# Performance work log

Hardware: AMD Instinct MI355X
Metric: run time of the kernel (lower is better)

## Reference

```python
import jax, jax.numpy as jnp
import numpy as np

EPS = 1e-10            # safe_log epsilon
SIGMOID_BETA = 1.0
MLE_STEP_SIZE = 0.01
NUM_MLE_STEPS = 15
ENT_MULT = 0.01        # entropy loss multiplier placeholder
DECAY_MULT = 0.001     # weight decay multiplier placeholder
B, P, N, T = 512, 1024, 1024, 32


def sigmoid(a, beta=SIGMOID_BETA):
    # module's rescaled sigmoid: 2/(1+exp(-beta*a)) - 1, range (-1, 1)
    return 2.0 / (1.0 + jnp.exp(-beta * a)) - 1.0


def tri_basis(a_sig, centers):
    # triangle basis functions: relu(1 - |a - c_j| / width), width = center spacing
    # a_sig [B,N], centers [T] -> [B,N,T]
    width = centers[1] - centers[0]
    return jax.nn.relu(1.0 - jnp.abs(a_sig[..., None] - centers) / width)


def prob_est(a_sig, thetas, centers):
    # per-neuron mixture of triangle kernels; mixture weights = softmax(thetas)
    pi = jax.nn.softmax(thetas, axis=1)               # [N,T]
    return jnp.einsum('bnt,nt->bn', tri_basis(a_sig, centers), pi)  # [B,N]


def log_likelihood(a_sig, thetas, centers):
    return jnp.sum(jnp.log(prob_est(a_sig, thetas, centers) + EPS))


def calc_entropy(probs):
    # per-neuron entropy reduction over the batch axis
    return -jnp.sum(probs * jnp.log(probs + EPS), axis=0)  # [N]


def setup_inputs() -> dict:
    key = jax.random.key(0)
    k0, k1, k2, k3 = jax.random.split(key, 4)
    x = jax.random.normal(k0, (B, P), jnp.float32)
    w_enc = 0.5 * jax.random.normal(k1, (P, N), jnp.float32)   # truncated_normal std 0.5 approx
    b_enc = 0.1 * jax.random.normal(k2, (N,), jnp.float32)
    w_dec = jnp.transpose(w_enc)                                # initialized as w_enc^T
    b_dec = 0.1 * jax.random.normal(k3, (P,), jnp.float32)
    thetas = jnp.ones((N, T), jnp.float32)                      # construct_thetas init
    triangle_centers = jnp.linspace(-1.0, 1.0, T).astype(jnp.float32)  # a_sig range
    return {"x": x, "w_enc": w_enc, "b_enc": b_enc, "w_dec": w_dec,
            "b_dec": b_dec, "thetas": thetas, "triangle_centers": triangle_centers}


def reference(x, w_enc, b_enc, w_dec, b_dec, thetas, triangle_centers):
    # --- inference: relu encoder (noise_var_mult = 0 -> deterministic a) ---
    a = jax.nn.relu(x @ w_enc + b_enc)                # [B,N]
    a_sig = sigmoid(a, SIGMOID_BETA)                  # [B,N] in (-1,1)

    # --- iterative MLE gradient-ascent on thetas (num_mle_steps updates) ---
    ll_grad = jax.grad(lambda th: log_likelihood(a_sig, th, triangle_centers))

    def mle_step(th, _):
        return th + MLE_STEP_SIZE * ll_grad(th), None

    thetas_new, _ = jax.lax.scan(mle_step, thetas, None, length=NUM_MLE_STEPS)

    # --- entropy of the triangle-kernel density estimate ---
    probs = prob_est(a_sig, thetas_new, triangle_centers)   # [B,N]
    a_entropies = calc_entropy(probs)                       # [N]

    # --- decoder / losses ---
    x_hat = a @ w_dec + b_dec                               # [B,P]
    recon_loss = jnp.mean(0.5 * jnp.sum((x - x_hat) ** 2, axis=1))
    entropy_loss = ENT_MULT * jnp.sum(a_entropies)
    # tf.nn.l2_loss(t) = sum(t^2)/2
    decay_loss = 0.5 * DECAY_MULT * (0.5 * jnp.sum(w_enc ** 2) + 0.5 * jnp.sum(w_dec ** 2))
    total_loss = recon_loss + entropy_loss + decay_loss
    return x_hat, a_entropies, total_loss
```

## Files before the change

kernel.cpp:

```cpp
#include <hip/hip_runtime.h>

#define EPSC 1e-10f
#define BDIM 512
#define PDIM 1024
#define NDIM 1024
#define TDIM 32

typedef __attribute__((ext_vector_type(8))) short short8;
typedef __attribute__((ext_vector_type(4))) float f32x4;
typedef __attribute__((ext_vector_type(2))) int int2v;

static __device__ __forceinline__ short f2bf(float f) {
  unsigned u = __float_as_uint(f);
  unsigned r = (u + 0x7fffu + ((u >> 16) & 1u)) >> 16;
  return (short)r;
}

template <int CTRL>
static __device__ __forceinline__ float dpp_add(float x) {
  int t = __builtin_amdgcn_update_dpp(0, __float_as_int(x), CTRL, 0xf, 0xf, true);
  return x + __int_as_float(t);
}
static __device__ __forceinline__ float sum16_all(float x) {
  x = dpp_add<0xB1>(x);
  x = dpp_add<0x4E>(x);
  x = dpp_add<0x141>(x);
  x = dpp_add<0x140>(x);
  return x;
}
static __device__ __forceinline__ float sum32_all(float x) {
  x = sum16_all(x);
  int2v r = __builtin_amdgcn_permlane16_swap(__float_as_int(x), __float_as_int(x), false, false);
  return __int_as_float(r[0]) + __int_as_float(r[1]);
}
static __device__ __forceinline__ float sum64_all(float x) {
  x = sum32_all(x);
  int2v r = __builtin_amdgcn_permlane32_swap(__float_as_int(x), __float_as_int(x), false, false);
  return __int_as_float(r[0]) + __int_as_float(r[1]);
}

__global__ __launch_bounds__(256) void conv_kernel(
    const float* __restrict__ X, short* __restrict__ Xbf,
    const float* __restrict__ W1, const float* __restrict__ W2,
    short* __restrict__ T1, short* __restrict__ T2, float* __restrict__ accums)
{
  __shared__ float T[64][65];
  __shared__ float red[4];
  int tid = threadIdx.x;
  int bid = blockIdx.x;
  if (bid < 256) {
    size_t base = (size_t)bid * 2048 + (size_t)tid * 8;
    float4 v0 = *(const float4*)(X + base);
    float4 v1 = *(const float4*)(X + base + 4);
    short8 o;
    o[0] = f2bf(v0.x); o[1] = f2bf(v0.y); o[2] = f2bf(v0.z); o[3] = f2bf(v0.w);
    o[4] = f2bf(v1.x); o[5] = f2bf(v1.y); o[6] = f2bf(v1.z); o[7] = f2bf(v1.w);
    *(short8*)(Xbf + base) = o;
    return;
  }
  int wbid = bid - 256;
  int z = wbid >> 8;
  int rem = wbid & 255;
  int r0 = (rem >> 4) * 64;
  int c0 = (rem & 15) * 64;
  const float* src = z ? W2 : W1;
  short* dst = z ? T2 : T1;
  float wsq = 0.0f;
#pragma unroll
  for (int i = 0; i < 4; ++i) {
    int row = (tid >> 4) + i * 16;
    int col = (tid & 15) << 2;
    float4 v = *(const float4*)(src + (size_t)(r0 + row) * NDIM + c0 + col);
    T[row][col + 0] = v.x; T[row][col + 1] = v.y; T[row][col + 2] = v.z; T[row][col + 3] = v.w;
    wsq = fmaf(v.x, v.x, wsq); wsq = fmaf(v.y, v.y, wsq);
    wsq = fmaf(v.z, v.z, wsq); wsq = fmaf(v.w, v.w, wsq);
  }
  __syncthreads();
  int n = tid >> 2;
  int kb = (tid & 3) << 4;
  short8 o0, o1;
#pragma unroll
  for (int i = 0; i < 8; ++i) o0[i] = f2bf(T[kb + i][n]);
#pragma unroll
  for (int i = 0; i < 8; ++i) o1[i] = f2bf(T[kb + 8 + i][n]);
  short* dp = dst + (size_t)(c0 + n) * NDIM + r0 + kb;
  *(short8*)dp = o0;
  *(short8*)(dp + 8) = o1;
  wsq = sum64_all(wsq);
  if ((tid & 63) == 0) red[tid >> 6] = wsq;
  __syncthreads();
  if (tid == 0) atomicAdd(accums + 2, red[0] + red[1] + red[2] + red[3]);
}

__global__ __launch_bounds__(512) void gemm1_mfma(
    const short* __restrict__ Xbf, const short* __restrict__ WT,
    const float* __restrict__ bias, const float* __restrict__ centers,
    short* __restrict__ Abf, float* __restrict__ U)
{
  __shared__ float red[4][64][9];
  int tid = threadIdx.x;
  int lane = tid & 63, wid = tid >> 6;
  int ow = wid & 3, kz = wid >> 2;
  int q = lane >> 4, r16 = lane & 15;
  int bn = blockIdx.x * 32;
  int m = blockIdx.y * 64 + ow * 16 + r16;
  const short* ap  = Xbf + (size_t)m * NDIM + kz * 512 + q * 8;
  const short* b0p = WT + (size_t)(bn + r16) * NDIM + kz * 512 + q * 8;
  const short* b1p = b0p + 16 * NDIM;
  f32x4 acc0 = {0.f, 0.f, 0.f, 0.f};
  f32x4 acc1 = {0.f, 0.f, 0.f, 0.f};
#pragma unroll 4
  for (int k = 0; k < 512; k += 32) {
    short8 a  = *(const short8*)(ap + k);
    short8 b0 = *(const short8*)(b0p + k);
    short8 b1 = *(const short8*)(b1p + k);
    acc0 = __builtin_amdgcn_mfma_f32_16x16x32_bf16(a, b0, acc0, 0, 0, 0);
    acc1 = __builtin_amdgcn_mfma_f32_16x16x32_bf16(a, b1, acc1, 0, 0, 0);
  }
  if (kz) {
#pragma unroll
    for (int r = 0; r < 4; ++r) { red[ow][lane][r] = acc0[r]; red[ow][lane][r + 4] = acc1[r]; }
  }
  __syncthreads();
  if (!kz) {
#pragma unroll
    for (int r = 0; r < 4; ++r) { acc0[r] += red[ow][lane][r]; acc1[r] += red[ow][lane][r + 4]; }
    float c0v = centers[0];
    float invw = 1.0f / (centers[1] - centers[0]);
    int mrow = blockIdx.y * 64 + ow * 16 + (q << 2);
    int n0 = bn + r16;
    float bi0 = bias[n0], bi1 = bias[n0 + 16];
    float u0[4], u1[4];
#pragma unroll
    for (int r = 0; r < 4; ++r) {
      int mm = mrow + r;
      float a0 = fmaxf(acc0[r] + bi0, 0.0f);
      float a1 = fmaxf(acc1[r] + bi1, 0.0f);
      Abf[(size_t)mm * NDIM + n0]      = f2bf(a0);
      Abf[(size_t)mm * NDIM + n0 + 16] = f2bf(a1);
      u0[r] = (2.0f * __builtin_amdgcn_rcpf(1.0f + __expf(-a0)) - 1.0f - c0v) * invw;
      u1[r] = (2.0f * __builtin_amdgcn_rcpf(1.0f + __expf(-a1)) - 1.0f - c0v) * invw;
    }
    *(float4*)(U + (size_t)n0 * BDIM + mrow)          = *(float4*)u0;
    *(float4*)(U + (size_t)(n0 + 16) * BDIM + mrow)   = *(float4*)u1;
  }
}

__global__ __launch_bounds__(512) void fused2_kernel(
    const short* __restrict__ Abf, const short* __restrict__ WdT,
    const float* __restrict__ b_dec, const float* __restrict__ X,
    const float* __restrict__ U, const float* __restrict__ thetas,
    float* __restrict__ out, float* __restrict__ ent_out, float* __restrict__ accums)
{
  __shared__ float smem[2312];
  int tid = threadIdx.x;
  int bx = blockIdx.x;
  if (bx < 256) {
    int lane = tid & 63, wid = tid >> 6;
    int ow = wid & 3, kz = wid >> 2;
    int q = lane >> 4, r16 = lane & 15;
    int bn = (bx & 31) * 32;
    int by = bx >> 5;
    int m = by * 64 + ow * 16 + r16;
    const short* ap  = Abf + (size_t)m * NDIM + kz * 512 + q * 8;
    const short* b0p = WdT + (size_t)(bn + r16) * NDIM + kz * 512 + q * 8;
    const short* b1p = b0p + 16 * NDIM;
    f32x4 acc0 = {0.f, 0.f, 0.f, 0.f};
    f32x4 acc1 = {0.f, 0.f, 0.f, 0.f};
#pragma unroll 4
    for (int k = 0; k < 512; k += 32) {
      short8 a  = *(const short8*)(ap + k);
      short8 b0 = *(const short8*)(b0p + k);
      short8 b1 = *(const short8*)(b1p + k);
      acc0 = __builtin_amdgcn_mfma_f32_16x16x32_bf16(a, b0, acc0, 0, 0, 0);
      acc1 = __builtin_amdgcn_mfma_f32_16x16x32_bf16(a, b1, acc1, 0, 0, 0);
    }
    float* rw = smem + ((ow * 64 + lane) * 9);
    if (kz) {
#pragma unroll
      for (int r = 0; r < 4; ++r) { rw[r] = acc0[r]; rw[r + 4] = acc1[r]; }
    }
    __syncthreads();
    float local = 0.0f;
    if (!kz) {
#pragma unroll
      for (int r = 0; r < 4; ++r) { acc0[r] += rw[r]; acc1[r] += rw[r + 4]; }
      int mrow = by * 64 + ow * 16 + (q << 2);
      int p0 = bn + r16;
      float bi0 = b_dec[p0], bi1 = b_dec[p0 + 16];
#pragma unroll
      for (int r = 0; r < 4; ++r) {
        int mm = mrow + r;
        float xh0 = acc0[r] + bi0;
        float xh1 = acc1[r] + bi1;
        out[(size_t)mm * PDIM + p0]      = xh0;
        out[(size_t)mm * PDIM + p0 + 16] = xh1;
        float d0 = xh0 - X[(size_t)mm * PDIM + p0];
        float d1 = xh1 - X[(size_t)mm * PDIM + p0 + 16];
        local = fmaf(d0, d0, local);
        local = fmaf(d1, d1, local);
      }
    }
    local = sum64_all(local);
    if ((tid & 63) == 0) smem[2304 + wid] = local;
    __syncthreads();
    if (tid == 0) {
      float s = 0.0f;
#pragma unroll
      for (int i = 0; i < 8; ++i) s += smem[2304 + i];
      atomicAdd(accums + 0, s);
    }
  } else {
    int wid = tid >> 6, lane = tid & 63;
    int n = (bx - 256) * 8 + wid;
    const float* Un = U + (size_t)n * BDIM;
    float u_reg[8], f_reg[8];
    int j_reg[8];
#pragma unroll
    for (int i = 0; i < 8; ++i) {
      float u = Un[lane + i * 64];
      int j = (int)u;
      if (j > TDIM - 2) j = TDIM - 2;
      u_reg[i] = u;
      j_reg[i] = j;
      f_reg[i] = u - (float)j;
    }
    float tv = thetas[(size_t)n * TDIM + (lane & 31)];
    int t = lane & 31;
    for (int step = 0; step < 15; ++step) {
      float e = __expf(tv - 1.0f);
      float se = sum32_all(e);
      float pv = e * __builtin_amdgcn_rcpf(se);
      float S = 0.0f;
      float cs[17];
#pragma unroll
      for (int k = 0; k < 17; ++k) cs[k] = 0.0f;
#pragma unroll
      for (int i = 0; i < 8; ++i) {
        float pj  = __shfl(pv, j_reg[i]);
        float pj1 = __shfl(pv, j_reg[i] + 1);
        float p = fmaf(f_reg[i], pj1 - pj, pj);
        float r = __builtin_amdgcn_rcpf(p + EPSC);
        S = fmaf(p, r, S);
        float u = u_reg[i];
#pragma unroll
        for (int k = 0; k < 17; ++k) {
          float w = __saturatef(1.0f - fabsf(u - (float)(15 + k)));
          cs[k] = fmaf(w, r, cs[k]);
        }
      }
      S = sum64_all(S);
#pragma unroll
      for (int k = 0; k < 17; ++k) cs[k] = sum64_all(cs[k]);
      float colsum = 0.0f;
#pragma unroll
      for (int k = 0; k < 17; ++k) colsum = (t == 15 + k) ? cs[k] : colsum;
      if (lane < 32) tv += 0.01f * pv * (colsum - S);
    }
    float e = __expf(tv - 1.0f);
    float se = sum32_all(e);
    float pv = e * __builtin_amdgcn_rcpf(se);
    float ent_local = 0.0f;
#pragma unroll
    for (int i = 0; i < 8; ++i) {
      float pj  = __shfl(pv, j_reg[i]);
      float pj1 = __shfl(pv, j_reg[i] + 1);
      float p = fmaf(f_reg[i], pj1 - pj, pj);
      ent_local = fmaf(p, __logf(p + EPSC), ent_local);
    }
    float E = sum64_all(ent_local);
    if (lane == 0) {
      float entn = -E;
      ent_out[n] = entn;
      atomicAdd(accums + 1, entn);
    }
  }
  __syncthreads();
  if (tid == 0) {
    __threadfence();
    float old = atomicAdd(accums + 3, 1.0f);
    if (old == 383.0f) {
      float recon = atomicAdd(accums + 0, 0.0f);
      float ent   = atomicAdd(accums + 1, 0.0f);
      float wsq   = atomicAdd(accums + 2, 0.0f);
      out[(size_t)BDIM * PDIM + NDIM] =
          recon * (0.5f / (float)BDIM) + 0.01f * ent + 0.00025f * wsq;
    }
  }
}

extern "C" void kernel_launch(void* const* d_in, const int* in_sizes, int n_in,
                              void* d_out, int out_size, void* d_ws, size_t ws_size,
                              hipStream_t stream) {
  (void)in_sizes; (void)n_in; (void)out_size; (void)ws_size;
  const float* x       = (const float*)d_in[0];
  const float* w_enc   = (const float*)d_in[1];
  const float* b_enc   = (const float*)d_in[2];
  const float* w_dec   = (const float*)d_in[3];
  const float* b_dec   = (const float*)d_in[4];
  const float* thetas  = (const float*)d_in[5];
  const float* centers = (const float*)d_in[6];
  float* out = (float*)d_out;

  char* ws = (char*)d_ws;
  short* Xbf    = (short*)(ws);
  short* WT     = (short*)(ws + (1 << 20));
  short* WdT    = (short*)(ws + (3 << 20));
  short* Abf    = (short*)(ws + (5 << 20));
  float* accums = (float*)(ws + (6 << 20));
  float* U      = (float*)(ws + (7 << 20));
  float* ent_out = out + (size_t)BDIM * PDIM;

  hipMemsetAsync(accums, 0, 16, stream);
  hipLaunchKernelGGL(conv_kernel, dim3(768), dim3(256), 0, stream,
                     x, Xbf, w_enc, w_dec, WT, WdT, accums);
  hipLaunchKernelGGL(gemm1_mfma, dim3(32, 8), dim3(512), 0, stream,
                     Xbf, WT, b_enc, centers, Abf, U);
  hipLaunchKernelGGL(fused2_kernel, dim3(384), dim3(512), 0, stream,
                     Abf, WdT, b_dec, x, U, thetas, out, ent_out, accums);
}
```

Baseline: 149.5 us.

## Spread MLE entropy work over more blocks and pack basis weights as float pairs

```diff
diff --git a/kernel.cpp b/kernel.cpp
--- a/kernel.cpp
+++ b/kernel.cpp
@@ -8,6 +8,7 @@
 
 typedef __attribute__((ext_vector_type(8))) short short8;
 typedef __attribute__((ext_vector_type(4))) float f32x4;
+typedef __attribute__((ext_vector_type(2))) float f32x2;
 typedef __attribute__((ext_vector_type(2))) int int2v;
 
 static __device__ __forceinline__ short f2bf(float f) {
@@ -212,74 +213,100 @@
     }
   } else {
     int wid = tid >> 6, lane = tid & 63;
-    int n = (bx - 256) * 8 + wid;
-    const float* Un = U + (size_t)n * BDIM;
-    float u_reg[8], f_reg[8];
-    int j_reg[8];
-#pragma unroll
-    for (int i = 0; i < 8; ++i) {
-      float u = Un[lane + i * 64];
-      int j = (int)u;
-      if (j > TDIM - 2) j = TDIM - 2;
-      u_reg[i] = u;
-      j_reg[i] = j;
-      f_reg[i] = u - (float)j;
-    }
-    float tv = thetas[(size_t)n * TDIM + (lane & 31)];
-    int t = lane & 31;
-    for (int step = 0; step < 15; ++step) {
+    if (wid < 4) {
+      int n = (bx - 256) * 4 + wid;
+      const float* Un = U + (size_t)n * BDIM;
+      float u_reg[8], f_reg[8];
+      int j_reg[8];
+#pragma unroll
+      for (int i = 0; i < 8; ++i) {
+        float u = Un[lane + i * 64];
+        int j = (int)u;
+        if (j > TDIM - 2) j = TDIM - 2;
+        u_reg[i] = u;
+        j_reg[i] = j;
+        f_reg[i] = u - (float)j;
+      }
+      f32x2 cpair[9];
+#pragma unroll
+      for (int k2 = 0; k2 < 9; ++k2) {
+        cpair[k2][0] = (float)(15 + 2 * k2);
+        cpair[k2][1] = (float)(16 + 2 * k2);
+      }
+      const f32x2 f2one  = {1.0f, 1.0f};
+      const f32x2 f2zero = {0.0f, 0.0f};
+      float tv = thetas[(size_t)n * TDIM + (lane & 31)];
+      int t = lane & 31;
+      for (int step = 0; step < 15; ++step) {
+        float e = __expf(tv - 1.0f);
+        float se = sum32_all(e);
+        float pv = e * __builtin_amdgcn_rcpf(se);
+        float pj[8], pj1[8];
+#pragma unroll
+        for (int i = 0; i < 8; ++i) {
+          pj[i]  = __shfl(pv, j_reg[i]);
+          pj1[i] = __shfl(pv, j_reg[i] + 1);
+        }
+        float rr[8];
+        float S = 0.0f;
+#pragma unroll
+        for (int i = 0; i < 8; ++i) {
+          float p = fmaf(f_reg[i], pj1[i] - pj[i], pj[i]);
+          rr[i] = __builtin_amdgcn_rcpf(p + EPSC);
+          S = fmaf(p, rr[i], S);
+        }
+        f32x2 cs2[9];
+#pragma unroll
+        for (int k2 = 0; k2 < 9; ++k2) cs2[k2] = f2zero;
+#pragma unroll
+        for (int i = 0; i < 8; ++i) {
+          f32x2 u2 = {u_reg[i], u_reg[i]};
+          f32x2 r2 = {rr[i], rr[i]};
+#pragma unroll
+          for (int k2 = 0; k2 < 9; ++k2) {
+            f32x2 d = u2 - cpair[k2];
+            f32x2 w = __builtin_elementwise_max(
+                f2one - __builtin_elementwise_abs(d), f2zero);
+            cs2[k2] = __builtin_elementwise_fma(w, r2, cs2[k2]);
+          }
+        }
+        S = sum64_all(S);
+        float colsum = 0.0f;
+#pragma unroll
+        for (int k = 0; k < 17; ++k) {
+          float cv = sum64_all(cs2[k >> 1][k & 1]);
+          colsum = (t == 15 + k) ? cv : colsum;
+        }
+        if (lane < 32) tv += 0.01f * pv * (colsum - S);
+      }
       float e = __expf(tv - 1.0f);
       float se = sum32_all(e);
       float pv = e * __builtin_amdgcn_rcpf(se);
-      float S = 0.0f;
-      float cs[17];
-#pragma unroll
-      for (int k = 0; k < 17; ++k) cs[k] = 0.0f;
+      float pj[8], pj1[8];
 #pragma unroll
       for (int i = 0; i < 8; ++i) {
-        float pj  = __shfl(pv, j_reg[i]);
-        float pj1 = __shfl(pv, j_reg[i] + 1);
-        float p = fmaf(f_reg[i], pj1 - pj, pj);
-        float r = __builtin_amdgcn_rcpf(p + EPSC);
-        S = fmaf(p, r, S);
-        float u = u_reg[i];
-#pragma unroll
-        for (int k = 0; k < 17; ++k) {
-          float w = __saturatef(1.0f - fabsf(u - (float)(15 + k)));
-          cs[k] = fmaf(w, r, cs[k]);
-        }
-      }
-      S = sum64_all(S);
-#pragma unroll
-      for (int k = 0; k < 17; ++k) cs[k] = sum64_all(cs[k]);
-      float colsum = 0.0f;
-#pragma unroll
-      for (int k = 0; k < 17; ++k) colsum = (t == 15 + k) ? cs[k] : colsum;
-      if (lane < 32) tv += 0.01f * pv * (colsum - S);
-    }
-    float e = __expf(tv - 1.0f);
-    float se = sum32_all(e);
-    float pv = e * __builtin_amdgcn_rcpf(se);
-    float ent_local = 0.0f;
-#pragma unroll
-    for (int i = 0; i < 8; ++i) {
-      float pj  = __shfl(pv, j_reg[i]);
-      float pj1 = __shfl(pv, j_reg[i] + 1);
-      float p = fmaf(f_reg[i], pj1 - pj, pj);
-      ent_local = fmaf(p, __logf(p + EPSC), ent_local);
-    }
-    float E = sum64_all(ent_local);
-    if (lane == 0) {
-      float entn = -E;
-      ent_out[n] = entn;
-      atomicAdd(accums + 1, entn);
+        pj[i]  = __shfl(pv, j_reg[i]);
+        pj1[i] = __shfl(pv, j_reg[i] + 1);
+      }
+      float ent_local = 0.0f;
+#pragma unroll
+      for (int i = 0; i < 8; ++i) {
+        float p = fmaf(f_reg[i], pj1[i] - pj[i], pj[i]);
+        ent_local = fmaf(p, __logf(p + EPSC), ent_local);
+      }
+      float E = sum64_all(ent_local);
+      if (lane == 0) {
+        float entn = -E;
+        ent_out[n] = entn;
+        atomicAdd(accums + 1, entn);
+      }
     }
   }
   __syncthreads();
   if (tid == 0) {
     __threadfence();
     float old = atomicAdd(accums + 3, 1.0f);
-    if (old == 383.0f) {
+    if (old == 511.0f) {
       float recon = atomicAdd(accums + 0, 0.0f);
       float ent   = atomicAdd(accums + 1, 0.0f);
       float wsq   = atomicAdd(accums + 2, 0.0f);
@@ -316,6 +343,6 @@
                      x, Xbf, w_enc, w_dec, WT, WdT, accums);
   hipLaunchKernelGGL(gemm1_mfma, dim3(32, 8), dim3(512), 0, stream,
                      Xbf, WT, b_enc, centers, Abf, U);
-  hipLaunchKernelGGL(fused2_kernel, dim3(384), dim3(512), 0, stream,
+  hipLaunchKernelGGL(fused2_kernel, dim3(512), dim3(512), 0, stream,
                      Abf, WdT, b_dec, x, U, thetas, out, ent_out, accums);
 }
```

Result: no change. 149.4 us (-0.1%).
